# Performance work log

Measured on AMD Instinct MI355X. Metric: run time of the kernel, lower is better.

The kernel has to match this reference:

```python
import jax, jax.numpy as jnp
import numpy as np
import math

C, HEADS = 128, 4
HD = C // HEADS
MID = max(C // 4, 8)

def _conv1x1(x, W, b):
    # x: (B?, C, H, W) ; W: (O, C) ; b: (O,)
    return jnp.einsum('bchw,oc->bohw', x, W) + b[None, :, None, None]

def _conv3x3(x, W, b):
    # W: (O, I, 3, 3), NCHW / OIHW, SAME padding
    y = jax.lax.conv_general_dilated(x, W, window_strides=(1, 1), padding='SAME',
                                     dimension_numbers=('NCHW', 'OIHW', 'NCHW'))
    return y + b[None, :, None, None]

def setup_inputs() -> dict:
    key = jax.random.key(0)
    ks = jax.random.split(key, 24)
    B, N, H, W = 4, 6, 128, 128
    s = 0.05
    inp = {
        'bev_views': jax.random.normal(ks[0], (B, N, C, H, W), jnp.float32),
        'snr_db': jax.random.normal(ks[1], (B, 1), jnp.float32) * 10.0,
        'view_reliability': jax.random.uniform(ks[2], (B, N, 3), jnp.float32),
        'Wq': jax.random.normal(ks[3], (C, C), jnp.float32) * s,
        'bq': jnp.zeros((C,), jnp.float32),
        'Wk': jax.random.normal(ks[4], (C, C), jnp.float32) * s,
        'bk': jnp.zeros((C,), jnp.float32),
        'Wv': jax.random.normal(ks[5], (C, C), jnp.float32) * s,
        'bv': jnp.zeros((C,), jnp.float32),
        'Wo1': jax.random.normal(ks[6], (C, C), jnp.float32) * s,
        'bo1': jnp.zeros((C,), jnp.float32),
        'Wo2': jax.random.normal(ks[7], (C, C, 3, 3), jnp.float32) * s,
        'bo2': jnp.zeros((C,), jnp.float32),
        'Wc1': jax.random.normal(ks[8], (MID, C), jnp.float32) * s,
        'bc1': jnp.zeros((MID,), jnp.float32),
        'Wc2': jax.random.normal(ks[9], (1, MID), jnp.float32) * s,
        'bc2': jnp.zeros((1,), jnp.float32),
        'Wg': jax.random.normal(ks[10], (C, 1), jnp.float32) * s,
        'bg': jnp.zeros((C,), jnp.float32),
        'Wr1': jax.random.normal(ks[11], (MID, 3), jnp.float32) * s,
        'br1': jnp.zeros((MID,), jnp.float32),
        'Wr2': jax.random.normal(ks[12], (1, MID), jnp.float32) * s,
        'br2': jnp.zeros((1,), jnp.float32),
    }
    return inp

def reference(bev_views, snr_db, view_reliability,
              Wq, bq, Wk, bk, Wv, bv, Wo1, bo1, Wo2, bo2,
              Wc1, bc1, Wc2, bc2, Wg, bg, Wr1, br1, Wr2, br2):
    B, N, Cc, H, W = bev_views.shape
    # --- cross-view semantic denoising (per-pixel cross-view attention) ---
    gq = bev_views.mean(axis=1)                       # (B,C,H,W)
    q = _conv1x1(gq, Wq, bq).reshape(B, HEADS, HD, H, W)
    flat = bev_views.reshape(B * N, Cc, H, W)
    k = _conv1x1(flat, Wk, bk).reshape(B, N, HEADS, HD, H, W)
    v = _conv1x1(flat, Wv, bv).reshape(B, N, HEADS, HD, H, W)
    # score over head_dim, softmax over views N
    score = jnp.einsum('bmdhw,bnmdhw->bnmhw', q, k) / math.sqrt(HD)
    attn = jax.nn.softmax(score, axis=1)              # (B,N,heads,H,W)
    fused = jnp.einsum('bnmhw,bnmdhw->bmdhw', attn, v).reshape(B, Cc, H, W)
    fused = _conv3x3(jax.nn.relu(_conv1x1(fused, Wo1, bo1)), Wo2, bo2) + gq
    attn_map = attn.mean(axis=2)                      # (B,N,H,W)
    # --- confidence-gated fusion ---
    conf = _conv1x1(jax.nn.relu(_conv1x1(flat, Wc1, bc1)), Wc2, bc2)
    conf_logits = conf.reshape(B, N, 1, H, W)
    rel_bias = (jax.nn.relu(view_reliability.reshape(B * N, 3) @ Wr1.T + br1) @ Wr2.T + br2)
    conf_logits = conf_logits + rel_bias.reshape(B, N, 1, 1, 1)
    conf_weights = jax.nn.softmax(conf_logits, axis=1)  # (B,N,1,H,W)
    fused_conf = (conf_weights * bev_views).sum(axis=1)  # (B,C,H,W)
    # --- SNR gate ---
    snr_norm = jnp.clip(snr_db / 20.0, -1.5, 1.5)       # (B,1)
    gate = jax.nn.sigmoid(snr_norm @ Wg.T + bg).reshape(B, Cc, 1, 1)
    out = gate * fused + (1.0 - gate) * fused_conf
    return (out, attn_map, conf_weights)
```

## Files before the change

### kernel.cpp

```cpp
#include <hip/hip_runtime.h>
#include <hip/hip_bf16.h>
#include <math.h>


#define BB   4
#define NV   6
#define CH   128
#define HGT  128
#define WID  128
#define MIDD 32
#define HWP  (HGT*WID)
#define TP   32

#define SWZ(pix) (((pix) & 15) << 3)

typedef __attribute__((ext_vector_type(8))) short bf16x8;
typedef __attribute__((ext_vector_type(4))) float f32x4;
typedef __attribute__((ext_vector_type(2))) unsigned int u32x2;

union U8 { bf16x8 v; unsigned u[4]; };

__device__ __forceinline__ ushort f2bf(float f) {
    union { __hip_bfloat16 h; ushort u; } v;
    v.h = __float2bfloat16(f);
    return v.u;
}
__device__ __forceinline__ float bf2f(ushort u) {
    return __uint_as_float(((unsigned)u) << 16);
}
__device__ __forceinline__ unsigned cvt_pk_bf16(float lo, float hi) {
    unsigned r;
    asm("v_cvt_pk_bf16_f32 %0, %1, %2" : "=v"(r) : "v"(lo), "v"(hi));
    return r;
}

__global__ void fusion_setup(const float* __restrict__ snr, const float* __restrict__ vr,
                             const float* __restrict__ Wg, const float* __restrict__ bg,
                             const float* __restrict__ Wr1, const float* __restrict__ br1,
                             const float* __restrict__ Wr2, const float* __restrict__ br2,
                             float* __restrict__ relb, float* __restrict__ gate)
{
    int tid = blockIdx.x * blockDim.x + threadIdx.x;
    if (tid < BB*CH) {
        int b = tid >> 7, c = tid & 127;
        float s = snr[b] * 0.05f;
        s = fminf(fmaxf(s, -1.5f), 1.5f);
        float z = s * Wg[c] + bg[c];
        gate[tid] = 1.0f / (1.0f + __expf(-z));
    }
    if (tid < BB*NV) {
        int b = tid / NV, n = tid % NV;
        float v0 = vr[(b*NV+n)*3+0], v1 = vr[(b*NV+n)*3+1], v2 = vr[(b*NV+n)*3+2];
        float acc = br2[0];
        for (int j = 0; j < MIDD; ++j) {
            float h = Wr1[j*3+0]*v0 + Wr1[j*3+1]*v1 + Wr1[j*3+2]*v2 + br1[j];
            acc += Wr2[j] * fmaxf(h, 0.0f);
        }
        relb[tid] = acc;
    }
}

__global__ void pack_weights(const float* __restrict__ Wq, const float* __restrict__ Wk,
                             const float* __restrict__ Wv, const float* __restrict__ Wo1,
                             const float* __restrict__ Wc1, const float* __restrict__ Wo2,
                             ushort* __restrict__ wqp, ushort* __restrict__ wkp,
                             ushort* __restrict__ wvp, ushort* __restrict__ wo1p,
                             ushort* __restrict__ wc1p, ushort* __restrict__ wo2p)
{
    int tid = blockIdx.x * 256 + threadIdx.x;
    if (tid >= 27136) return;
    if (tid < 8192) {
        int m = tid >> 11;
        int local = tid & 2047;
        const float* src = (m == 0) ? Wq : (m == 1) ? Wk : (m == 2) ? Wv : Wo1;
        ushort* dst = (m == 0) ? wqp : (m == 1) ? wkp : (m == 2) ? wvp : wo1p;
        int ks = local >> 9, rem = local & 511;
        int nf = rem >> 6, lane = rem & 63;
        int o = nf*16 + (lane & 15);
        int i0 = ks*32 + ((lane >> 4) << 3);
        const float* s = src + o*CH + i0;
        ushort* d = dst + local*8;
#pragma unroll
        for (int j = 0; j < 8; ++j) d[j] = f2bf(s[j]);
    } else if (tid < 8704) {
        int local = tid - 8192;
        int ks = local >> 7, rem = local & 127;
        int nf = rem >> 6, lane = rem & 63;
        int o = nf*16 + (lane & 15);
        int i0 = ks*32 + ((lane >> 4) << 3);
        const float* s = Wc1 + o*CH + i0;
        ushort* d = wc1p + local*8;
#pragma unroll
        for (int j = 0; j < 8; ++j) d[j] = f2bf(s[j]);
    } else {
        int l2 = tid - 8704;
        int lane = l2 & 63;
        int rest = l2 >> 6;
        int nf = rest & 7;
        int kst = rest >> 3;
        int ks = kst & 3;
        int tap = kst >> 2;
        int co = nf*16 + (lane & 15);
        int ci0 = ks*32 + ((lane >> 4) << 3);
        ushort* d = wo2p + l2*8;
#pragma unroll
        for (int j = 0; j < 8; ++j) d[j] = f2bf(Wo2[(co*CH + ci0 + j)*9 + tap]);
    }
}

__device__ __forceinline__ bf16x8 ldsA(const ushort* tile, int lane, int mf, int ks) {
    int pix = mf*16 + (lane & 15);
    int idx = (pix*128 + ks*32 + ((lane >> 4) << 3)) ^ SWZ(pix);
    return *(const bf16x8*)(tile + idx);
}
__device__ __forceinline__ bf16x8 ldB(const ushort* pack, int lane, int ks, int nf, int NF) {
    return *(const bf16x8*)(pack + (((ks*NF + nf)*64) + lane)*8);
}

__global__ __launch_bounds__(256, 3) void fusion_attn(
    const float* __restrict__ bev,
    const ushort* __restrict__ wqp, const ushort* __restrict__ wkp,
    const ushort* __restrict__ wvp, const ushort* __restrict__ wo1p,
    const ushort* __restrict__ wc1p,
    const float* __restrict__ bq, const float* __restrict__ bk,
    const float* __restrict__ bv, const float* __restrict__ bo1,
    const float* __restrict__ bc1, const float* __restrict__ bc2,
    const float* __restrict__ Wc2, const float* __restrict__ relb,
    ushort* __restrict__ gq_bf, ushort* __restrict__ t_bf, ushort* __restrict__ fc_bf,
    float* __restrict__ attn_o, float* __restrict__ conf_o)
{
    __shared__ ushort xt[NV][TP*128];
    __shared__ float  scat[NV][4][TP];
    __shared__ float  dnm[4][TP];
    __shared__ float  lpart[NV][TP];
    __shared__ float  cfw[NV][TP];

    const int t = threadIdx.x, lane = t & 63, w = t >> 6;
    const int vb = ((blockIdx.x & 7) << 8) | (blockIdx.x >> 3);
    const int b = vb >> 9;
    const int pix0 = (vb & 511) * TP;

    const int pixg = (t & 3) * 8;
    const int c0   = (t >> 2) * 2;
    const float* sb = bev + (((size_t)b*NV*CH + c0)*HWP + pix0 + pixg);
    const size_t vstep = (size_t)CH*HWP;
    float gacc[16];
#pragma unroll
    for (int i = 0; i < 16; ++i) gacc[i] = 0.f;
    float4 L[NV][4];
#pragma unroll
    for (int j = 0; j < NV; ++j) {
        const float* s1 = sb + (size_t)j*vstep;
        L[j][0] = *(const float4*)(s1);
        L[j][1] = *(const float4*)(s1 + 4);
        L[j][2] = *(const float4*)(s1 + HWP);
        L[j][3] = *(const float4*)(s1 + HWP + 4);
    }
#pragma unroll
    for (int n = 0; n < NV; ++n) {
        float4 a0 = L[n][0], a1 = L[n][1], b0 = L[n][2], b1 = L[n][3];
        float r0[8] = {a0.x,a0.y,a0.z,a0.w, a1.x,a1.y,a1.z,a1.w};
        float r1[8] = {b0.x,b0.y,b0.z,b0.w, b1.x,b1.y,b1.z,b1.w};
#pragma unroll
        for (int p = 0; p < 8; ++p) {
            int pix = pixg + p;
            unsigned pk = cvt_pk_bf16(r0[p], r1[p]);
            *(unsigned*)(&xt[n][(pix*128 + c0) ^ SWZ(pix)]) = pk;
            gacc[p]   += r0[p];
            gacc[8+p] += r1[p];
        }
    }
    {
        U8 g0, g1;
#pragma unroll
        for (int p = 0; p < 4; ++p) {
            g0.u[p] = cvt_pk_bf16(gacc[2*p]   * (1.0f/6.0f), gacc[2*p+1] * (1.0f/6.0f));
            g1.u[p] = cvt_pk_bf16(gacc[8+2*p] * (1.0f/6.0f), gacc[9+2*p] * (1.0f/6.0f));
        }
        ushort* gd = gq_bf + ((size_t)(b*CH + c0)*HWP + pix0 + pixg);
        *(bf16x8*)(gd)       = g0.v;
        *(bf16x8*)(gd + HWP) = g1.v;
    }
    __syncthreads();

    const int cl0 = (lane & 15);
    const int rg  = (lane >> 4) << 2;

    f32x4 qf[2][2];
#pragma unroll
    for (int mf = 0; mf < 2; ++mf)
#pragma unroll
        for (int nfl = 0; nfl < 2; ++nfl) qf[mf][nfl] = (f32x4){0.f,0.f,0.f,0.f};
#pragma unroll 2
    for (int n = 0; n < NV; ++n) {
        bf16x8 xA[2][4];
#pragma unroll
        for (int mf = 0; mf < 2; ++mf)
#pragma unroll
            for (int ks = 0; ks < 4; ++ks) xA[mf][ks] = ldsA(xt[n], lane, mf, ks);
#pragma unroll
        for (int nfl = 0; nfl < 2; ++nfl) {
#pragma unroll
            for (int ks = 0; ks < 4; ++ks) {
                bf16x8 bb = ldB(wqp, lane, ks, 2*w + nfl, 8);
#pragma unroll
                for (int mf = 0; mf < 2; ++mf)
                    qf[mf][nfl] = __builtin_amdgcn_mfma_f32_16x16x32_bf16(bb, xA[mf][ks], qf[mf][nfl], 0, 0, 0);
            }
        }
        if (n == w || n == w + 4) {
            f32x4 cf[2][2];
#pragma unroll
            for (int mf = 0; mf < 2; ++mf)
#pragma unroll
                for (int nfc = 0; nfc < 2; ++nfc) cf[mf][nfc] = (f32x4){0.f,0.f,0.f,0.f};
#pragma unroll
            for (int nfc = 0; nfc < 2; ++nfc) {
#pragma unroll
                for (int ks = 0; ks < 4; ++ks) {
                    bf16x8 bb = ldB(wc1p, lane, ks, nfc, 2);
#pragma unroll
                    for (int mf = 0; mf < 2; ++mf)
                        cf[mf][nfc] = __builtin_amdgcn_mfma_f32_16x16x32_bf16(bb, xA[mf][ks], cf[mf][nfc], 0, 0, 0);
                }
            }
            const f32x4 bc1T0 = *(const f32x4*)(bc1 + rg),  bc1T1 = *(const f32x4*)(bc1 + 16 + rg);
            const f32x4 wc2T0 = *(const f32x4*)(Wc2 + rg),  wc2T1 = *(const f32x4*)(Wc2 + 16 + rg);
#pragma unroll
            for (int mf = 0; mf < 2; ++mf) {
                float pl = 0.f;
#pragma unroll
                for (int r = 0; r < 4; ++r) {
                    pl += fmaxf(cf[mf][0][r] + bc1T0[r], 0.f) * wc2T0[r];
                    pl += fmaxf(cf[mf][1][r] + bc1T1[r], 0.f) * wc2T1[r];
                }
                pl += __shfl_xor(pl, 16, 64);
                pl += __shfl_xor(pl, 32, 64);
                if (lane < 16) lpart[n][mf*16 + lane] = pl;
            }
        }
    }
    {
        const f32x4 bqT0 = *(const f32x4*)(bq + w*32 + rg), bqT1 = *(const f32x4*)(bq + w*32 + 16 + rg);
#pragma unroll
        for (int mf = 0; mf < 2; ++mf)
#pragma unroll
            for (int r = 0; r < 4; ++r) {
                qf[mf][0][r] = qf[mf][0][r]*(1.0f/6.0f) + bqT0[r];
                qf[mf][1][r] = qf[mf][1][r]*(1.0f/6.0f) + bqT1[r];
            }
    }

    float sb2[2];
    {
        const f32x4 bkT0 = *(const f32x4*)(bk + w*32 + rg), bkT1 = *(const f32x4*)(bk + w*32 + 16 + rg);
#pragma unroll
        for (int mf = 0; mf < 2; ++mf) {
            float v = 0.f;
#pragma unroll
            for (int r = 0; r < 4; ++r) {
                v += qf[mf][0][r]*bkT0[r];
                v += qf[mf][1][r]*bkT1[r];
            }
            sb2[mf] = v;
        }
    }
    float denom[2] = {0.f, 0.f};
#pragma unroll 2
    for (int n = 0; n < NV; ++n) {
        bf16x8 xA[2][4];
#pragma unroll
        for (int mf = 0; mf < 2; ++mf)
#pragma unroll
            for (int ks = 0; ks < 4; ++ks) xA[mf][ks] = ldsA(xt[n], lane, mf, ks);
        f32x4 kf[2][2];
#pragma unroll
        for (int mf = 0; mf < 2; ++mf)
#pragma unroll
            for (int nfl = 0; nfl < 2; ++nfl) kf[mf][nfl] = (f32x4){0.f,0.f,0.f,0.f};
#pragma unroll
        for (int nfl = 0; nfl < 2; ++nfl)
#pragma unroll
            for (int ks = 0; ks < 4; ++ks) {
                bf16x8 bb = ldB(wkp, lane, ks, 2*w + nfl, 8);
#pragma unroll
                for (int mf = 0; mf < 2; ++mf)
                    kf[mf][nfl] = __builtin_amdgcn_mfma_f32_16x16x32_bf16(bb, xA[mf][ks], kf[mf][nfl], 0, 0, 0);
            }
#pragma unroll
        for (int mf = 0; mf < 2; ++mf) {
            float s = sb2[mf];
#pragma unroll
            for (int r = 0; r < 4; ++r) {
                s += qf[mf][0][r]*kf[mf][0][r];
                s += qf[mf][1][r]*kf[mf][1][r];
            }
            s += __shfl_xor(s, 16, 64);
            s += __shfl_xor(s, 32, 64);
            float e = __expf(s * 0.17677669529663687f);
            denom[mf] += e;
            if (lane < 16) scat[n][w][mf*16 + lane] = e;
        }
    }
    const float inv0 = 1.0f/denom[0], inv1 = 1.0f/denom[1];
    if (lane < 32) dnm[w][lane] = (lane & 16) ? inv1 : inv0;

    f32x4 ff[2][2];
#pragma unroll
    for (int mf = 0; mf < 2; ++mf)
#pragma unroll
        for (int nfl = 0; nfl < 2; ++nfl) ff[mf][nfl] = (f32x4){0.f,0.f,0.f,0.f};
#pragma unroll 2
    for (int n = 0; n < NV; ++n) {
        bf16x8 xA[2][4];
#pragma unroll
        for (int mf = 0; mf < 2; ++mf)
#pragma unroll
            for (int ks = 0; ks < 4; ++ks) xA[mf][ks] = ldsA(xt[n], lane, mf, ks);
        f32x4 vv[2][2];
#pragma unroll
        for (int mf = 0; mf < 2; ++mf)
#pragma unroll
            for (int nfl = 0; nfl < 2; ++nfl) vv[mf][nfl] = (f32x4){0.f,0.f,0.f,0.f};
#pragma unroll
        for (int nfl = 0; nfl < 2; ++nfl)
#pragma unroll
            for (int ks = 0; ks < 4; ++ks) {
                bf16x8 bb = ldB(wvp, lane, ks, 2*w + nfl, 8);
#pragma unroll
                for (int mf = 0; mf < 2; ++mf)
                    vv[mf][nfl] = __builtin_amdgcn_mfma_f32_16x16x32_bf16(bb, xA[mf][ks], vv[mf][nfl], 0, 0, 0);
            }
        float a0 = scat[n][w][cl0]      * inv0;
        float a1 = scat[n][w][16 + cl0] * inv1;
#pragma unroll
        for (int r = 0; r < 4; ++r) {
            ff[0][0][r] += a0 * vv[0][0][r];
            ff[0][1][r] += a0 * vv[0][1][r];
            ff[1][0][r] += a1 * vv[1][0][r];
            ff[1][1][r] += a1 * vv[1][1][r];
        }
    }
    {
        const f32x4 bvT0 = *(const f32x4*)(bv + w*32 + rg), bvT1 = *(const f32x4*)(bv + w*32 + 16 + rg);
#pragma unroll
        for (int mf = 0; mf < 2; ++mf)
#pragma unroll
            for (int r = 0; r < 4; ++r) { ff[mf][0][r] += bvT0[r]; ff[mf][1][r] += bvT1[r]; }
    }
    __syncthreads();

    if (t < 32) {
        int pix = t;
        float bc2v = bc2[0];
        float lg[NV];
#pragma unroll
        for (int n = 0; n < NV; ++n)
            lg[n] = lpart[n][pix] + bc2v + relb[b*NV + n];
        float mx = fmaxf(fmaxf(fmaxf(lg[0],lg[1]),fmaxf(lg[2],lg[3])),fmaxf(lg[4],lg[5]));
        float e[NV], sum = 0.f;
#pragma unroll
        for (int n = 0; n < NV; ++n) { e[n] = __expf(lg[n]-mx); sum += e[n]; }
        float inv = 1.0f/sum;
#pragma unroll
        for (int n = 0; n < NV; ++n) {
            float wv = e[n]*inv;
            cfw[n][pix] = wv;
            conf_o[(b*NV + n)*HWP + pix0 + pix] = wv;
        }
    }
    if (t < 192) {
        int n = t >> 5, pix = t & 31;
        float am = 0.25f*(scat[n][0][pix]*dnm[0][pix] + scat[n][1][pix]*dnm[1][pix]
                        + scat[n][2][pix]*dnm[2][pix] + scat[n][3][pix]*dnm[3][pix]);
        attn_o[(b*NV + n)*HWP + pix0 + pix] = am;
    }
    __syncthreads();

    {
        float fcv[16];
#pragma unroll
        for (int i = 0; i < 16; ++i) fcv[i] = 0.f;
#pragma unroll
        for (int n = 0; n < NV; ++n) {
#pragma unroll
            for (int p = 0; p < 8; ++p) {
                int pix = pixg + p;
                float cwv = cfw[n][pix];
                unsigned pk = *(const unsigned*)(&xt[n][(pix*128 + c0) ^ SWZ(pix)]);
                fcv[p]   += cwv * bf2f((ushort)(pk & 0xffffu));
                fcv[8+p] += cwv * bf2f((ushort)(pk >> 16));
            }
        }
        U8 f0, f1;
#pragma unroll
        for (int p = 0; p < 4; ++p) {
            f0.u[p] = cvt_pk_bf16(fcv[2*p],   fcv[2*p+1]);
            f1.u[p] = cvt_pk_bf16(fcv[8+2*p], fcv[9+2*p]);
        }
        ushort* fd = fc_bf + ((size_t)(b*CH + c0)*HWP + pix0 + pixg);
        *(bf16x8*)(fd)       = f0.v;
        *(bf16x8*)(fd + HWP) = f1.v;
    }
    __syncthreads();

    {
        ushort* xt0 = &xt[0][0];
#pragma unroll
        for (int mf = 0; mf < 2; ++mf)
#pragma unroll
            for (int nfl = 0; nfl < 2; ++nfl) {
                int pix = mf*16 + cl0;
                int c   = w*32 + nfl*16 + rg;
                unsigned lo = cvt_pk_bf16(ff[mf][nfl][0], ff[mf][nfl][1]);
                unsigned hi = cvt_pk_bf16(ff[mf][nfl][2], ff[mf][nfl][3]);
                *(u32x2*)(&xt0[(pix*128 + c) ^ SWZ(pix)]) = (u32x2){lo, hi};
            }
    }
    __syncthreads();

    {
        bf16x8 aA[2][4];
#pragma unroll
        for (int mf = 0; mf < 2; ++mf)
#pragma unroll
            for (int ks = 0; ks < 4; ++ks) aA[mf][ks] = ldsA(&xt[0][0], lane, mf, ks);
        f32x4 tf[2][2];
#pragma unroll
        for (int mf = 0; mf < 2; ++mf)
#pragma unroll
            for (int nfl = 0; nfl < 2; ++nfl) tf[mf][nfl] = (f32x4){0.f,0.f,0.f,0.f};
#pragma unroll
        for (int nfl = 0; nfl < 2; ++nfl) {
            int nf = 2*w + nfl;
#pragma unroll
            for (int ks = 0; ks < 4; ++ks) {
                bf16x8 bb = ldB(wo1p, lane, ks, nf, 8);
#pragma unroll
                for (int mf = 0; mf < 2; ++mf)
                    tf[mf][nfl] = __builtin_amdgcn_mfma_f32_16x16x32_bf16(aA[mf][ks], bb, tf[mf][nfl], 0, 0, 0);
            }
        }
        const float bov0 = bo1[w*32 + cl0], bov1 = bo1[w*32 + 16 + cl0];
#pragma unroll
        for (int mf = 0; mf < 2; ++mf)
#pragma unroll
            for (int nfl = 0; nfl < 2; ++nfl)
#pragma unroll
                for (int r = 0; r < 4; ++r) {
                    int pix = mf*16 + rg + r;
                    int c   = w*32 + nfl*16 + cl0;
                    float bo_ = nfl ? bov1 : bov0;
                    t_bf[(size_t)(b*HWP + pix0 + pix)*128 + c] = f2bf(fmaxf(tf[mf][nfl][r] + bo_, 0.f));
                }
    }
}

__global__ __launch_bounds__(256, 2) void fusion_conv3(
    const ushort* __restrict__ t_bf, const ushort* __restrict__ gq_bf,
    const ushort* __restrict__ fc_bf, const ushort* __restrict__ wo2p,
    const float* __restrict__ bo2, const float* __restrict__ gate,
    float* __restrict__ out)
{
    __shared__ ushort halo[10*34*64];

    const int t = threadIdx.x, lane = t & 63, w = t >> 6;
    const int vbk = ((blockIdx.x & 7) << 6) | (blockIdx.x >> 3);
    const int cg   = vbk & 1;
    const int tile = (vbk >> 1) & 63;
    const int b    = vbk >> 7;
    const int h0 = (tile >> 2) * 8;
    const int w0 = (tile & 3) * 32;

    const int c8   = (t & 7) * 8;
    const int cell0 = t >> 3;

    for (int i = cell0; i < 340; i += 32) {
        int r = i / 34, cc = i - r*34;
        int hs = h0 - 1 + r, wsr = w0 - 1 + cc;
        bf16x8 v = (bf16x8){0,0,0,0,0,0,0,0};
        if ((unsigned)hs < (unsigned)HGT && (unsigned)wsr < (unsigned)WID)
            v = *(const bf16x8*)(t_bf + ((size_t)(b*HWP + hs*WID + wsr)*128 + c8));
        *(bf16x8*)(&halo[(i*64 + c8) ^ ((cc & 7) << 3)]) = v;
    }
    bf16x8 stg[11];
#pragma unroll
    for (int j = 0; j < 11; ++j) {
        int i = cell0 + 32*j;
        if (i < 340) {
            int r = i / 34, cc = i - r*34;
            int hs = h0 - 1 + r, wsr = w0 - 1 + cc;
            bf16x8 v = (bf16x8){0,0,0,0,0,0,0,0};
            if ((unsigned)hs < (unsigned)HGT && (unsigned)wsr < (unsigned)WID)
                v = *(const bf16x8*)(t_bf + ((size_t)(b*HWP + hs*WID + wsr)*128 + 64 + c8));
            stg[j] = v;
        }
    }
    __syncthreads();

    f32x4 acc[4][4];
#pragma unroll
    for (int mi = 0; mi < 4; ++mi)
#pragma unroll
        for (int nfl = 0; nfl < 4; ++nfl) acc[mi][nfl] = (f32x4){0.f,0.f,0.f,0.f};

    const int mcol = lane & 15;
    const int koff = (lane >> 4) << 3;

#pragma unroll 1
    for (int k = 0; k < 2; ++k) {
#pragma unroll 1
        for (int tap = 0; tap < 9; ++tap) {
            const int dy = tap / 3, dx = tap - dy*3;
            const int col = mcol + dx;
            const int swz = (col & 7) << 3;
#pragma unroll
            for (int ks2 = 0; ks2 < 2; ++ks2) {
                bf16x8 Bf[4];
#pragma unroll
                for (int nfl = 0; nfl < 4; ++nfl)
                    Bf[nfl] = *(const bf16x8*)(wo2p + (((size_t)((tap*4 + k*2 + ks2)*8 + cg*4 + nfl))*64 + lane)*8);
#pragma unroll
                for (int mi = 0; mi < 4; ++mi) {
                    int mf = w*4 + mi;
                    int r_ = mf >> 1, g = mf & 1;
                    int idx = ((((r_ + dy)*34 + g*16 + col))*64 + ks2*32 + koff) ^ swz;
                    bf16x8 Af = *(const bf16x8*)(&halo[idx]);
#pragma unroll
                    for (int nfl = 0; nfl < 4; ++nfl)
                        acc[mi][nfl] = __builtin_amdgcn_mfma_f32_16x16x32_bf16(Af, Bf[nfl], acc[mi][nfl], 0, 0, 0);
                }
            }
        }
        if (k == 0) {
            __syncthreads();
#pragma unroll
            for (int j = 0; j < 11; ++j) {
                int i = cell0 + 32*j;
                if (i < 340) {
                    int cc = i % 34;
                    *(bf16x8*)(&halo[(i*64 + c8) ^ ((cc & 7) << 3)]) = stg[j];
                }
            }
            __syncthreads();
        }
    }

    float* fbuf = (float*)halo;
    const int cl0 = lane & 15;
    const int rg  = (lane >> 4) << 2;
    const int c32 = t & 31;
    const int row8 = t >> 5;
#pragma unroll 1
    for (int sp = 0; sp < 2; ++sp) {
        __syncthreads();
#pragma unroll
        for (int mi = 0; mi < 4; ++mi)
#pragma unroll
            for (int nl = 0; nl < 2; ++nl) {
                int nfl = sp*2 + nl;
                int mf = w*4 + mi;
                int pix = (mf >> 1)*32 + (mf & 1)*16 + rg;
                *(f32x4*)(fbuf + (nl*16 + cl0)*260 + pix) = acc[mi][nfl];
            }
        __syncthreads();
        {
            const int c  = cg*64 + sp*32 + c32;
            const float gt  = gate[b*CH + c];
            const float gti = 1.0f - gt;
            const float b2v = bo2[c];
            const int gbase = (b*CH + c)*HWP + (h0 + row8)*WID + w0;
            float* od = out + gbase;
#pragma unroll
            for (int q = 0; q < 4; ++q) {
                f32x4 cv0 = *(const f32x4*)(fbuf + c32*260 + row8*32 + q*8);
                f32x4 cv1 = *(const f32x4*)(fbuf + c32*260 + row8*32 + q*8 + 4);
                bf16x8 gq8 = *(const bf16x8*)(gq_bf + gbase + q*8);
                bf16x8 fc8 = *(const bf16x8*)(fc_bf + gbase + q*8);
                float vv[8];
#pragma unroll
                for (int jj = 0; jj < 4; ++jj) {
                    vv[jj]   = gt*(cv0[jj] + b2v + bf2f((ushort)gq8[jj]))   + gti*bf2f((ushort)fc8[jj]);
                    vv[4+jj] = gt*(cv1[jj] + b2v + bf2f((ushort)gq8[4+jj])) + gti*bf2f((ushort)fc8[4+jj]);
                }
                *(float4*)(od + q*8)     = (float4){vv[0],vv[1],vv[2],vv[3]};
                *(float4*)(od + q*8 + 4) = (float4){vv[4],vv[5],vv[6],vv[7]};
            }
        }
    }
}

extern "C" void kernel_launch(void* const* d_in, const int* in_sizes, int n_in,
                              void* d_out, int out_size, void* d_ws, size_t ws_size,
                              hipStream_t stream)
{
    const float* bev = (const float*)d_in[0];
    const float* snr = (const float*)d_in[1];
    const float* vr  = (const float*)d_in[2];
    const float* Wq  = (const float*)d_in[3];
    const float* bq  = (const float*)d_in[4];
    const float* Wk  = (const float*)d_in[5];
    const float* bk  = (const float*)d_in[6];
    const float* Wv  = (const float*)d_in[7];
    const float* bv  = (const float*)d_in[8];
    const float* Wo1 = (const float*)d_in[9];
    const float* bo1 = (const float*)d_in[10];
    const float* Wo2 = (const float*)d_in[11];
    const float* bo2 = (const float*)d_in[12];
    const float* Wc1 = (const float*)d_in[13];
    const float* bc1 = (const float*)d_in[14];
    const float* Wc2 = (const float*)d_in[15];
    const float* bc2 = (const float*)d_in[16];
    const float* Wg  = (const float*)d_in[17];
    const float* bg  = (const float*)d_in[18];
    const float* Wr1 = (const float*)d_in[19];
    const float* br1 = (const float*)d_in[20];
    const float* Wr2 = (const float*)d_in[21];
    const float* br2 = (const float*)d_in[22];

    char* wsb = (char*)d_ws;
    ushort* t_bf  = (ushort*)(wsb);
    ushort* gq_bf = (ushort*)(wsb + 16777216);
    ushort* fc_bf = (ushort*)(wsb + 33554432);
    ushort* wqp   = (ushort*)(wsb + 50331648);
    ushort* wkp   = wqp + 16384;
    ushort* wvp   = wkp + 16384;
    ushort* wo1p  = wvp + 16384;
    ushort* wc1p  = wo1p + 16384;
    ushort* wo2p  = wc1p + 4096;
    float*  gate  = (float*)(wsb + 50331648 + 434176);
    float*  relb  = gate + 512;

    float* outp   = (float*)d_out;
    float* attn_o = outp + 8388608;
    float* conf_o = outp + 8781824;

    fusion_setup<<<2, 256, 0, stream>>>(snr, vr, Wg, bg, Wr1, br1, Wr2, br2,
                                        relb, gate);
    pack_weights<<<106, 256, 0, stream>>>(Wq, Wk, Wv, Wo1, Wc1, Wo2,
                                          wqp, wkp, wvp, wo1p, wc1p, wo2p);
    fusion_attn<<<2048, 256, 0, stream>>>(bev, wqp, wkp, wvp, wo1p, wc1p,
                                          bq, bk, bv, bo1, bc1, bc2, Wc2, relb,
                                          gq_bf, t_bf, fc_bf, attn_o, conf_o);
    fusion_conv3<<<512, 256, 0, stream>>>(t_bf, gq_bf, fc_bf, wo2p, bo2, gate, outp);
}
```

Before: 148.0 us.

## Compute query projection once from view-mean instead of summing six per-view GEMMs

The query projection used to be accumulated over all six views with MFMA and then scaled by 1/6. It now uses linearity: the already-computed fp32 view mean is packed to bf16 into a small LDS buffer, in two 16-pixel halves that share storage with the scalar scratch arrays, and multiplied by Wq once. This removes about five sixths of the Q-projection MFMA work and the per-view A loads, at the cost of extra barriers and some LDS staging. The conf-head loop now visits only the views each warp owns.

```diff
diff --git a/kernel.cpp b/kernel.cpp
--- a/kernel.cpp
+++ b/kernel.cpp
@@ -130,10 +130,15 @@
     float* __restrict__ attn_o, float* __restrict__ conf_o)
 {
     __shared__ ushort xt[NV][TP*128];
-    __shared__ float  scat[NV][4][TP];
-    __shared__ float  dnm[4][TP];
-    __shared__ float  lpart[NV][TP];
-    __shared__ float  cfw[NV][TP];
+    __shared__ union {
+        struct {
+            float scat[NV][4][TP];
+            float dnm[4][TP];
+            float lpart[NV][TP];
+            float cfw[NV][TP];
+        } s;
+        ushort gqh[16*128];
+    } aux;
 
     const int t = threadIdx.x, lane = t & 63, w = t >> 6;
     const int vb = ((blockIdx.x & 7) << 8) | (blockIdx.x >> 3);
@@ -181,6 +186,14 @@
         *(bf16x8*)(gd)       = g0.v;
         *(bf16x8*)(gd + HWP) = g1.v;
     }
+    if ((t & 3) < 2) {
+#pragma unroll
+        for (int p = 0; p < 8; ++p) {
+            int pix = pixg + p;
+            unsigned pk = cvt_pk_bf16(gacc[p]*(1.0f/6.0f), gacc[8+p]*(1.0f/6.0f));
+            *(unsigned*)(&aux.gqh[((pix & 15)*128 + c0) ^ SWZ(pix)]) = pk;
+        }
+    }
     __syncthreads();
 
     const int cl0 = (lane & 15);
@@ -191,24 +204,49 @@
     for (int mf = 0; mf < 2; ++mf)
 #pragma unroll
         for (int nfl = 0; nfl < 2; ++nfl) qf[mf][nfl] = (f32x4){0.f,0.f,0.f,0.f};
-#pragma unroll 2
-    for (int n = 0; n < NV; ++n) {
-        bf16x8 xA[2][4];
-#pragma unroll
-        for (int mf = 0; mf < 2; ++mf)
-#pragma unroll
-            for (int ks = 0; ks < 4; ++ks) xA[mf][ks] = ldsA(xt[n], lane, mf, ks);
-#pragma unroll
-        for (int nfl = 0; nfl < 2; ++nfl) {
-#pragma unroll
-            for (int ks = 0; ks < 4; ++ks) {
-                bf16x8 bb = ldB(wqp, lane, ks, 2*w + nfl, 8);
-#pragma unroll
-                for (int mf = 0; mf < 2; ++mf)
-                    qf[mf][nfl] = __builtin_amdgcn_mfma_f32_16x16x32_bf16(bb, xA[mf][ks], qf[mf][nfl], 0, 0, 0);
-            }
-        }
-        if (n == w || n == w + 4) {
+    {
+        bf16x8 xg[4];
+#pragma unroll
+        for (int ks = 0; ks < 4; ++ks) xg[ks] = ldsA(aux.gqh, lane, 0, ks);
+#pragma unroll
+        for (int nfl = 0; nfl < 2; ++nfl)
+#pragma unroll
+            for (int ks = 0; ks < 4; ++ks)
+                qf[0][nfl] = __builtin_amdgcn_mfma_f32_16x16x32_bf16(
+                    ldB(wqp, lane, ks, 2*w + nfl, 8), xg[ks], qf[0][nfl], 0, 0, 0);
+    }
+    __syncthreads();
+    if ((t & 3) >= 2) {
+#pragma unroll
+        for (int p = 0; p < 8; ++p) {
+            int pix = pixg + p;
+            unsigned pk = cvt_pk_bf16(gacc[p]*(1.0f/6.0f), gacc[8+p]*(1.0f/6.0f));
+            *(unsigned*)(&aux.gqh[((pix & 15)*128 + c0) ^ SWZ(pix)]) = pk;
+        }
+    }
+    __syncthreads();
+    {
+        bf16x8 xg[4];
+#pragma unroll
+        for (int ks = 0; ks < 4; ++ks) xg[ks] = ldsA(aux.gqh, lane, 0, ks);
+#pragma unroll
+        for (int nfl = 0; nfl < 2; ++nfl)
+#pragma unroll
+            for (int ks = 0; ks < 4; ++ks)
+                qf[1][nfl] = __builtin_amdgcn_mfma_f32_16x16x32_bf16(
+                    ldB(wqp, lane, ks, 2*w + nfl, 8), xg[ks], qf[1][nfl], 0, 0, 0);
+    }
+    __syncthreads();
+
+#pragma unroll
+    for (int vi = 0; vi < 2; ++vi) {
+        int n = w + vi*4;
+        if (n < NV) {
+            bf16x8 xA[2][4];
+#pragma unroll
+            for (int mf = 0; mf < 2; ++mf)
+#pragma unroll
+                for (int ks = 0; ks < 4; ++ks) xA[mf][ks] = ldsA(xt[n], lane, mf, ks);
             f32x4 cf[2][2];
 #pragma unroll
             for (int mf = 0; mf < 2; ++mf)
@@ -236,7 +274,7 @@
                 }
                 pl += __shfl_xor(pl, 16, 64);
                 pl += __shfl_xor(pl, 32, 64);
-                if (lane < 16) lpart[n][mf*16 + lane] = pl;
+                if (lane < 16) aux.s.lpart[n][mf*16 + lane] = pl;
             }
         }
     }
@@ -246,8 +284,8 @@
         for (int mf = 0; mf < 2; ++mf)
 #pragma unroll
             for (int r = 0; r < 4; ++r) {
-                qf[mf][0][r] = qf[mf][0][r]*(1.0f/6.0f) + bqT0[r];
-                qf[mf][1][r] = qf[mf][1][r]*(1.0f/6.0f) + bqT1[r];
+                qf[mf][0][r] = qf[mf][0][r] + bqT0[r];
+                qf[mf][1][r] = qf[mf][1][r] + bqT1[r];
             }
     }
 
@@ -299,11 +337,11 @@
             s += __shfl_xor(s, 32, 64);
             float e = __expf(s * 0.17677669529663687f);
             denom[mf] += e;
-            if (lane < 16) scat[n][w][mf*16 + lane] = e;
+            if (lane < 16) aux.s.scat[n][w][mf*16 + lane] = e;
         }
     }
     const float inv0 = 1.0f/denom[0], inv1 = 1.0f/denom[1];
-    if (lane < 32) dnm[w][lane] = (lane & 16) ? inv1 : inv0;
+    if (lane < 32) aux.s.dnm[w][lane] = (lane & 16) ? inv1 : inv0;
 
     f32x4 ff[2][2];
 #pragma unroll
@@ -331,8 +369,8 @@
                 for (int mf = 0; mf < 2; ++mf)
                     vv[mf][nfl] = __builtin_amdgcn_mfma_f32_16x16x32_bf16(bb, xA[mf][ks], vv[mf][nfl], 0, 0, 0);
             }
-        float a0 = scat[n][w][cl0]      * inv0;
-        float a1 = scat[n][w][16 + cl0] * inv1;
+        float a0 = aux.s.scat[n][w][cl0]      * inv0;
+        float a1 = aux.s.scat[n][w][16 + cl0] * inv1;
 #pragma unroll
         for (int r = 0; r < 4; ++r) {
             ff[0][0][r] += a0 * vv[0][0][r];
@@ -356,7 +394,7 @@
         float lg[NV];
 #pragma unroll
         for (int n = 0; n < NV; ++n)
-            lg[n] = lpart[n][pix] + bc2v + relb[b*NV + n];
+            lg[n] = aux.s.lpart[n][pix] + bc2v + relb[b*NV + n];
         float mx = fmaxf(fmaxf(fmaxf(lg[0],lg[1]),fmaxf(lg[2],lg[3])),fmaxf(lg[4],lg[5]));
         float e[NV], sum = 0.f;
 #pragma unroll
@@ -365,14 +403,14 @@
 #pragma unroll
         for (int n = 0; n < NV; ++n) {
             float wv = e[n]*inv;
-            cfw[n][pix] = wv;
+            aux.s.cfw[n][pix] = wv;
             conf_o[(b*NV + n)*HWP + pix0 + pix] = wv;
         }
     }
     if (t < 192) {
         int n = t >> 5, pix = t & 31;
-        float am = 0.25f*(scat[n][0][pix]*dnm[0][pix] + scat[n][1][pix]*dnm[1][pix]
-                        + scat[n][2][pix]*dnm[2][pix] + scat[n][3][pix]*dnm[3][pix]);
+        float am = 0.25f*(aux.s.scat[n][0][pix]*aux.s.dnm[0][pix] + aux.s.scat[n][1][pix]*aux.s.dnm[1][pix]
+                        + aux.s.scat[n][2][pix]*aux.s.dnm[2][pix] + aux.s.scat[n][3][pix]*aux.s.dnm[3][pix]);
         attn_o[(b*NV + n)*HWP + pix0 + pix] = am;
     }
     __syncthreads();
@@ -386,7 +424,7 @@
 #pragma unroll
             for (int p = 0; p < 8; ++p) {
                 int pix = pixg + p;
-                float cwv = cfw[n][pix];
+                float cwv = aux.s.cfw[n][pix];
                 unsigned pk = *(const unsigned*)(&xt[n][(pix*128 + c0) ^ SWZ(pix)]);
                 fcv[p]   += cwv * bf2f((ushort)(pk & 0xffffu));
                 fcv[8+p] += cwv * bf2f((ushort)(pk >> 16));
```

Result: faster. 142.7 us (-3.6%).

## Halve view LDS tiles, compute Q from mean input, stream views in two halves

Applied to the files above, without the earlier changes.

The per-view bf16 LDS buffer shrinks from six views to three, and launch bounds move from 3 to 4 blocks per CU. Views 0-2 are processed first, then views 3-5 are reloaded from global into the same buffers, and views 0-2 are re-read from global for the confidence-weighted sum. Q is now computed once from the view mean held in a new LDS tile instead of accumulating Q over all six views. Softmax normalisation is deferred to the end, K/V passes are fused per view, and the swizzle gains extra XOR bits. The aim is more occupancy and fewer MFMAs, at the cost of extra global reads and more barriers.

```diff
diff --git a/kernel.cpp b/kernel.cpp
--- a/kernel.cpp
+++ b/kernel.cpp
@@ -12,7 +12,7 @@
 #define HWP  (HGT*WID)
 #define TP   32
 
-#define SWZ(pix) (((pix) & 15) << 3)
+#define SWZ(pix) ((((pix) & 15) << 3) ^ (((pix) & 24) << 1))
 
 typedef __attribute__((ext_vector_type(8))) short bf16x8;
 typedef __attribute__((ext_vector_type(4))) float f32x4;
@@ -117,7 +117,49 @@
     return *(const bf16x8*)(pack + (((ks*NF + nf)*64) + lane)*8);
 }
 
-__global__ __launch_bounds__(256, 3) void fusion_attn(
+__device__ __forceinline__ void conf_one(const ushort* xtile, int n, int lane, int rg,
+                                         const ushort* __restrict__ wc1p,
+                                         const float* __restrict__ bc1,
+                                         const float* __restrict__ Wc2,
+                                         float (*lpart)[TP])
+{
+    bf16x8 xA[2][4];
+#pragma unroll
+    for (int mf = 0; mf < 2; ++mf)
+#pragma unroll
+        for (int ks = 0; ks < 4; ++ks) xA[mf][ks] = ldsA(xtile, lane, mf, ks);
+    f32x4 cf[2][2];
+#pragma unroll
+    for (int mf = 0; mf < 2; ++mf)
+#pragma unroll
+        for (int nfc = 0; nfc < 2; ++nfc) cf[mf][nfc] = (f32x4){0.f,0.f,0.f,0.f};
+#pragma unroll
+    for (int nfc = 0; nfc < 2; ++nfc) {
+#pragma unroll
+        for (int ks = 0; ks < 4; ++ks) {
+            bf16x8 bb = ldB(wc1p, lane, ks, nfc, 2);
+#pragma unroll
+            for (int mf = 0; mf < 2; ++mf)
+                cf[mf][nfc] = __builtin_amdgcn_mfma_f32_16x16x32_bf16(bb, xA[mf][ks], cf[mf][nfc], 0, 0, 0);
+        }
+    }
+    const f32x4 bc1T0 = *(const f32x4*)(bc1 + rg),  bc1T1 = *(const f32x4*)(bc1 + 16 + rg);
+    const f32x4 wc2T0 = *(const f32x4*)(Wc2 + rg),  wc2T1 = *(const f32x4*)(Wc2 + 16 + rg);
+#pragma unroll
+    for (int mf = 0; mf < 2; ++mf) {
+        float pl = 0.f;
+#pragma unroll
+        for (int r = 0; r < 4; ++r) {
+            pl += fmaxf(cf[mf][0][r] + bc1T0[r], 0.f) * wc2T0[r];
+            pl += fmaxf(cf[mf][1][r] + bc1T1[r], 0.f) * wc2T1[r];
+        }
+        pl += __shfl_xor(pl, 16, 64);
+        pl += __shfl_xor(pl, 32, 64);
+        if (lane < 16) lpart[n][mf*16 + lane] = pl;
+    }
+}
+
+__global__ __launch_bounds__(256, 4) void fusion_attn(
     const float* __restrict__ bev,
     const ushort* __restrict__ wqp, const ushort* __restrict__ wkp,
     const ushort* __restrict__ wvp, const ushort* __restrict__ wo1p,
@@ -129,7 +171,8 @@
     ushort* __restrict__ gq_bf, ushort* __restrict__ t_bf, ushort* __restrict__ fc_bf,
     float* __restrict__ attn_o, float* __restrict__ conf_o)
 {
-    __shared__ ushort xt[NV][TP*128];
+    __shared__ ushort xt[3][TP*128];
+    __shared__ ushort gqh[TP*128];
     __shared__ float  scat[NV][4][TP];
     __shared__ float  dnm[4][TP];
     __shared__ float  lpart[NV][TP];
@@ -147,27 +190,31 @@
     float gacc[16];
 #pragma unroll
     for (int i = 0; i < 16; ++i) gacc[i] = 0.f;
-    float4 L[NV][4];
-#pragma unroll
-    for (int j = 0; j < NV; ++j) {
-        const float* s1 = sb + (size_t)j*vstep;
-        L[j][0] = *(const float4*)(s1);
-        L[j][1] = *(const float4*)(s1 + 4);
-        L[j][2] = *(const float4*)(s1 + HWP);
-        L[j][3] = *(const float4*)(s1 + HWP + 4);
-    }
-#pragma unroll
-    for (int n = 0; n < NV; ++n) {
-        float4 a0 = L[n][0], a1 = L[n][1], b0 = L[n][2], b1 = L[n][3];
-        float r0[8] = {a0.x,a0.y,a0.z,a0.w, a1.x,a1.y,a1.z,a1.w};
-        float r1[8] = {b0.x,b0.y,b0.z,b0.w, b1.x,b1.y,b1.z,b1.w};
-#pragma unroll
-        for (int p = 0; p < 8; ++p) {
-            int pix = pixg + p;
-            unsigned pk = cvt_pk_bf16(r0[p], r1[p]);
-            *(unsigned*)(&xt[n][(pix*128 + c0) ^ SWZ(pix)]) = pk;
-            gacc[p]   += r0[p];
-            gacc[8+p] += r1[p];
+    {
+        float4 L[NV][4];
+#pragma unroll
+        for (int j = 0; j < NV; ++j) {
+            const float* s1 = sb + (size_t)j*vstep;
+            L[j][0] = *(const float4*)(s1);
+            L[j][1] = *(const float4*)(s1 + 4);
+            L[j][2] = *(const float4*)(s1 + HWP);
+            L[j][3] = *(const float4*)(s1 + HWP + 4);
+        }
+#pragma unroll
+        for (int n = 0; n < NV; ++n) {
+            float4 a0 = L[n][0], a1 = L[n][1], b0 = L[n][2], b1 = L[n][3];
+            float r0[8] = {a0.x,a0.y,a0.z,a0.w, a1.x,a1.y,a1.z,a1.w};
+            float r1[8] = {b0.x,b0.y,b0.z,b0.w, b1.x,b1.y,b1.z,b1.w};
+#pragma unroll
+            for (int p = 0; p < 8; ++p) {
+                int pix = pixg + p;
+                if (n < 3) {
+                    unsigned pk = cvt_pk_bf16(r0[p], r1[p]);
+                    *(unsigned*)(&xt[n][(pix*128 + c0) ^ SWZ(pix)]) = pk;
+                }
+                gacc[p]   += r0[p];
+                gacc[8+p] += r1[p];
+            }
         }
     }
     {
@@ -181,6 +228,12 @@
         *(bf16x8*)(gd)       = g0.v;
         *(bf16x8*)(gd + HWP) = g1.v;
     }
+#pragma unroll
+    for (int p = 0; p < 8; ++p) {
+        int pix = pixg + p;
+        unsigned pk = cvt_pk_bf16(gacc[p]*(1.0f/6.0f), gacc[8+p]*(1.0f/6.0f));
+        *(unsigned*)(&gqh[(pix*128 + c0) ^ SWZ(pix)]) = pk;
+    }
     __syncthreads();
 
     const int cl0 = (lane & 15);
@@ -191,54 +244,17 @@
     for (int mf = 0; mf < 2; ++mf)
 #pragma unroll
         for (int nfl = 0; nfl < 2; ++nfl) qf[mf][nfl] = (f32x4){0.f,0.f,0.f,0.f};
-#pragma unroll 2
-    for (int n = 0; n < NV; ++n) {
-        bf16x8 xA[2][4];
-#pragma unroll
-        for (int mf = 0; mf < 2; ++mf)
-#pragma unroll
-            for (int ks = 0; ks < 4; ++ks) xA[mf][ks] = ldsA(xt[n], lane, mf, ks);
-#pragma unroll
-        for (int nfl = 0; nfl < 2; ++nfl) {
-#pragma unroll
-            for (int ks = 0; ks < 4; ++ks) {
-                bf16x8 bb = ldB(wqp, lane, ks, 2*w + nfl, 8);
-#pragma unroll
-                for (int mf = 0; mf < 2; ++mf)
-                    qf[mf][nfl] = __builtin_amdgcn_mfma_f32_16x16x32_bf16(bb, xA[mf][ks], qf[mf][nfl], 0, 0, 0);
-            }
-        }
-        if (n == w || n == w + 4) {
-            f32x4 cf[2][2];
-#pragma unroll
-            for (int mf = 0; mf < 2; ++mf)
-#pragma unroll
-                for (int nfc = 0; nfc < 2; ++nfc) cf[mf][nfc] = (f32x4){0.f,0.f,0.f,0.f};
-#pragma unroll
-            for (int nfc = 0; nfc < 2; ++nfc) {
-#pragma unroll
-                for (int ks = 0; ks < 4; ++ks) {
-                    bf16x8 bb = ldB(wc1p, lane, ks, nfc, 2);
-#pragma unroll
-                    for (int mf = 0; mf < 2; ++mf)
-                        cf[mf][nfc] = __builtin_amdgcn_mfma_f32_16x16x32_bf16(bb, xA[mf][ks], cf[mf][nfc], 0, 0, 0);
-                }
-            }
-            const f32x4 bc1T0 = *(const f32x4*)(bc1 + rg),  bc1T1 = *(const f32x4*)(bc1 + 16 + rg);
-            const f32x4 wc2T0 = *(const f32x4*)(Wc2 + rg),  wc2T1 = *(const f32x4*)(Wc2 + 16 + rg);
-#pragma unroll
-            for (int mf = 0; mf < 2; ++mf) {
-                float pl = 0.f;
-#pragma unroll
-                for (int r = 0; r < 4; ++r) {
-                    pl += fmaxf(cf[mf][0][r] + bc1T0[r], 0.f) * wc2T0[r];
-                    pl += fmaxf(cf[mf][1][r] + bc1T1[r], 0.f) * wc2T1[r];
-                }
-                pl += __shfl_xor(pl, 16, 64);
-                pl += __shfl_xor(pl, 32, 64);
-                if (lane < 16) lpart[n][mf*16 + lane] = pl;
-            }
-        }
+#pragma unroll
+    for (int mf = 0; mf < 2; ++mf) {
+        bf16x8 xg[4];
+#pragma unroll
+        for (int ks = 0; ks < 4; ++ks) xg[ks] = ldsA(gqh, lane, mf, ks);
+#pragma unroll
+        for (int nfl = 0; nfl < 2; ++nfl)
+#pragma unroll
+            for (int ks = 0; ks < 4; ++ks)
+                qf[mf][nfl] = __builtin_amdgcn_mfma_f32_16x16x32_bf16(
+                    ldB(wqp, lane, ks, 2*w + nfl, 8), xg[ks], qf[mf][nfl], 0, 0, 0);
     }
     {
         const f32x4 bqT0 = *(const f32x4*)(bq + w*32 + rg), bqT1 = *(const f32x4*)(bq + w*32 + 16 + rg);
@@ -246,11 +262,10 @@
         for (int mf = 0; mf < 2; ++mf)
 #pragma unroll
             for (int r = 0; r < 4; ++r) {
-                qf[mf][0][r] = qf[mf][0][r]*(1.0f/6.0f) + bqT0[r];
-                qf[mf][1][r] = qf[mf][1][r]*(1.0f/6.0f) + bqT1[r];
-            }
-    }
-
+                qf[mf][0][r] = qf[mf][0][r] + bqT0[r];
+                qf[mf][1][r] = qf[mf][1][r] + bqT1[r];
+            }
+    }
     float sb2[2];
     {
         const f32x4 bkT0 = *(const f32x4*)(bk + w*32 + rg), bkT1 = *(const f32x4*)(bk + w*32 + 16 + rg);
@@ -265,9 +280,17 @@
             sb2[mf] = v;
         }
     }
+
+    if (w < 3) conf_one(xt[w], w, lane, rg, wc1p, bc1, Wc2, lpart);
+
     float denom[2] = {0.f, 0.f};
-#pragma unroll 2
-    for (int n = 0; n < NV; ++n) {
+    f32x4 ff[2][2];
+#pragma unroll
+    for (int mf = 0; mf < 2; ++mf)
+#pragma unroll
+        for (int nfl = 0; nfl < 2; ++nfl) ff[mf][nfl] = (f32x4){0.f,0.f,0.f,0.f};
+#pragma unroll
+    for (int n = 0; n < 3; ++n) {
         bf16x8 xA[2][4];
 #pragma unroll
         for (int mf = 0; mf < 2; ++mf)
@@ -301,22 +324,6 @@
             denom[mf] += e;
             if (lane < 16) scat[n][w][mf*16 + lane] = e;
         }
-    }
-    const float inv0 = 1.0f/denom[0], inv1 = 1.0f/denom[1];
-    if (lane < 32) dnm[w][lane] = (lane & 16) ? inv1 : inv0;
-
-    f32x4 ff[2][2];
-#pragma unroll
-    for (int mf = 0; mf < 2; ++mf)
-#pragma unroll
-        for (int nfl = 0; nfl < 2; ++nfl) ff[mf][nfl] = (f32x4){0.f,0.f,0.f,0.f};
-#pragma unroll 2
-    for (int n = 0; n < NV; ++n) {
-        bf16x8 xA[2][4];
-#pragma unroll
-        for (int mf = 0; mf < 2; ++mf)
-#pragma unroll
-            for (int ks = 0; ks < 4; ++ks) xA[mf][ks] = ldsA(xt[n], lane, mf, ks);
         f32x4 vv[2][2];
 #pragma unroll
         for (int mf = 0; mf < 2; ++mf)
@@ -331,8 +338,8 @@
                 for (int mf = 0; mf < 2; ++mf)
                     vv[mf][nfl] = __builtin_amdgcn_mfma_f32_16x16x32_bf16(bb, xA[mf][ks], vv[mf][nfl], 0, 0, 0);
             }
-        float a0 = scat[n][w][cl0]      * inv0;
-        float a1 = scat[n][w][16 + cl0] * inv1;
+        float a0 = scat[n][w][cl0];
+        float a1 = scat[n][w][16 + cl0];
 #pragma unroll
         for (int r = 0; r < 4; ++r) {
             ff[0][0][r] += a0 * vv[0][0][r];
@@ -341,12 +348,106 @@
             ff[1][1][r] += a1 * vv[1][1][r];
         }
     }
+    __syncthreads();
+
+    {
+        float4 M[3][4];
+#pragma unroll
+        for (int j = 0; j < 3; ++j) {
+            const float* s1 = sb + (size_t)(j+3)*vstep;
+            M[j][0] = *(const float4*)(s1);
+            M[j][1] = *(const float4*)(s1 + 4);
+            M[j][2] = *(const float4*)(s1 + HWP);
+            M[j][3] = *(const float4*)(s1 + HWP + 4);
+        }
+#pragma unroll
+        for (int j = 0; j < 3; ++j) {
+            float4 a0 = M[j][0], a1 = M[j][1], b0 = M[j][2], b1 = M[j][3];
+            float r0[8] = {a0.x,a0.y,a0.z,a0.w, a1.x,a1.y,a1.z,a1.w};
+            float r1[8] = {b0.x,b0.y,b0.z,b0.w, b1.x,b1.y,b1.z,b1.w};
+#pragma unroll
+            for (int p = 0; p < 8; ++p) {
+                int pix = pixg + p;
+                unsigned pk = cvt_pk_bf16(r0[p], r1[p]);
+                *(unsigned*)(&xt[j][(pix*128 + c0) ^ SWZ(pix)]) = pk;
+            }
+        }
+    }
+    __syncthreads();
+
+    if (w == 3) conf_one(xt[0], 3, lane, rg, wc1p, bc1, Wc2, lpart);
+    if (w < 2)  conf_one(xt[w + 1], w + 4, lane, rg, wc1p, bc1, Wc2, lpart);
+
+#pragma unroll
+    for (int n = 3; n < NV; ++n) {
+        bf16x8 xA[2][4];
+#pragma unroll
+        for (int mf = 0; mf < 2; ++mf)
+#pragma unroll
+            for (int ks = 0; ks < 4; ++ks) xA[mf][ks] = ldsA(xt[n-3], lane, mf, ks);
+        f32x4 kf[2][2];
+#pragma unroll
+        for (int mf = 0; mf < 2; ++mf)
+#pragma unroll
+            for (int nfl = 0; nfl < 2; ++nfl) kf[mf][nfl] = (f32x4){0.f,0.f,0.f,0.f};
+#pragma unroll
+        for (int nfl = 0; nfl < 2; ++nfl)
+#pragma unroll
+            for (int ks = 0; ks < 4; ++ks) {
+                bf16x8 bb = ldB(wkp, lane, ks, 2*w + nfl, 8);
+#pragma unroll
+                for (int mf = 0; mf < 2; ++mf)
+                    kf[mf][nfl] = __builtin_amdgcn_mfma_f32_16x16x32_bf16(bb, xA[mf][ks], kf[mf][nfl], 0, 0, 0);
+            }
+#pragma unroll
+        for (int mf = 0; mf < 2; ++mf) {
+            float s = sb2[mf];
+#pragma unroll
+            for (int r = 0; r < 4; ++r) {
+                s += qf[mf][0][r]*kf[mf][0][r];
+                s += qf[mf][1][r]*kf[mf][1][r];
+            }
+            s += __shfl_xor(s, 16, 64);
+            s += __shfl_xor(s, 32, 64);
+            float e = __expf(s * 0.17677669529663687f);
+            denom[mf] += e;
+            if (lane < 16) scat[n][w][mf*16 + lane] = e;
+        }
+        f32x4 vv[2][2];
+#pragma unroll
+        for (int mf = 0; mf < 2; ++mf)
+#pragma unroll
+            for (int nfl = 0; nfl < 2; ++nfl) vv[mf][nfl] = (f32x4){0.f,0.f,0.f,0.f};
+#pragma unroll
+        for (int nfl = 0; nfl < 2; ++nfl)
+#pragma unroll
+            for (int ks = 0; ks < 4; ++ks) {
+                bf16x8 bb = ldB(wvp, lane, ks, 2*w + nfl, 8);
+#pragma unroll
+                for (int mf = 0; mf < 2; ++mf)
+                    vv[mf][nfl] = __builtin_amdgcn_mfma_f32_16x16x32_bf16(bb, xA[mf][ks], vv[mf][nfl], 0, 0, 0);
+            }
+        float a0 = scat[n][w][cl0];
+        float a1 = scat[n][w][16 + cl0];
+#pragma unroll
+        for (int r = 0; r < 4; ++r) {
+            ff[0][0][r] += a0 * vv[0][0][r];
+            ff[0][1][r] += a0 * vv[0][1][r];
+            ff[1][0][r] += a1 * vv[1][0][r];
+            ff[1][1][r] += a1 * vv[1][1][r];
+        }
+    }
+    const float inv0 = 1.0f/denom[0], inv1 = 1.0f/denom[1];
+    if (lane < 32) dnm[w][lane] = (lane & 16) ? inv1 : inv0;
     {
         const f32x4 bvT0 = *(const f32x4*)(bv + w*32 + rg), bvT1 = *(const f32x4*)(bv + w*32 + 16 + rg);
 #pragma unroll
-        for (int mf = 0; mf < 2; ++mf)
-#pragma unroll
-            for (int r = 0; r < 4; ++r) { ff[mf][0][r] += bvT0[r]; ff[mf][1][r] += bvT1[r]; }
+        for (int r = 0; r < 4; ++r) {
+            ff[0][0][r] = ff[0][0][r]*inv0 + bvT0[r];
+            ff[0][1][r] = ff[0][1][r]*inv0 + bvT1[r];
+            ff[1][0][r] = ff[1][0][r]*inv1 + bvT0[r];
+            ff[1][1][r] = ff[1][1][r]*inv1 + bvT1[r];
+        }
     }
     __syncthreads();
 
@@ -381,13 +482,36 @@
         float fcv[16];
 #pragma unroll
         for (int i = 0; i < 16; ++i) fcv[i] = 0.f;
-#pragma unroll
-        for (int n = 0; n < NV; ++n) {
+        {
+            float4 G[3][4];
+#pragma unroll
+            for (int j = 0; j < 3; ++j) {
+                const float* s1 = sb + (size_t)j*vstep;
+                G[j][0] = *(const float4*)(s1);
+                G[j][1] = *(const float4*)(s1 + 4);
+                G[j][2] = *(const float4*)(s1 + HWP);
+                G[j][3] = *(const float4*)(s1 + HWP + 4);
+            }
+#pragma unroll
+            for (int n = 0; n < 3; ++n) {
+                float4 a0 = G[n][0], a1 = G[n][1], b0 = G[n][2], b1 = G[n][3];
+                float r0[8] = {a0.x,a0.y,a0.z,a0.w, a1.x,a1.y,a1.z,a1.w};
+                float r1[8] = {b0.x,b0.y,b0.z,b0.w, b1.x,b1.y,b1.z,b1.w};
+#pragma unroll
+                for (int p = 0; p < 8; ++p) {
+                    float cwv = cfw[n][pixg + p];
+                    fcv[p]   += cwv * r0[p];
+                    fcv[8+p] += cwv * r1[p];
+                }
+            }
+        }
+#pragma unroll
+        for (int n = 3; n < NV; ++n) {
 #pragma unroll
             for (int p = 0; p < 8; ++p) {
                 int pix = pixg + p;
                 float cwv = cfw[n][pix];
-                unsigned pk = *(const unsigned*)(&xt[n][(pix*128 + c0) ^ SWZ(pix)]);
+                unsigned pk = *(const unsigned*)(&xt[n-3][(pix*128 + c0) ^ SWZ(pix)]);
                 fcv[p]   += cwv * bf2f((ushort)(pk & 0xffffu));
                 fcv[8+p] += cwv * bf2f((ushort)(pk >> 16));
             }
```

After: 351.9 us. 138% more time.
